# Performance work log

Measured on AMD Instinct MI355X. Metric: run time of the kernel, lower is better.

Reference implementation:

```python
import jax, jax.numpy as jnp
import numpy as np

T_, N_, DIN, D, HEADS, WW, E_, DPE = 8, 20000, 128, 128, 4, 4, 320000, 8
DH = D // HEADS
NEG = -1e30
EPS_GATE = 1e-6


def setup_inputs() -> dict:
    key = jax.random.key(0)
    ks = jax.random.split(key, 10)
    return {
        "H_tilde": jax.random.normal(ks[0], (T_, N_, DIN), jnp.float32),
        "S": jax.random.uniform(ks[1], (T_, N_), jnp.float32),
        "Wq": jax.random.normal(ks[2], (D, DIN), jnp.float32) * 0.05,
        "Wkh": jax.random.normal(ks[3], (D, DIN), jnp.float32) * 0.05,
        "Wkpe": jax.random.normal(ks[4], (D, DPE), jnp.float32) * 0.05,
        "Wv": jax.random.normal(ks[5], (D, DIN), jnp.float32) * 0.05,
        "pe_table": jax.random.normal(ks[6], (WW + 1, DPE), jnp.float32),
        "rel_bias": jax.random.normal(ks[7], (WW + 1,), jnp.float32),
        "src": jax.random.randint(ks[8], (E_,), 0, N_),
        "dst": jax.random.randint(ks[9], (E_,), 0, N_),
    }


def reference(H_tilde, S, Wq, Wkh, Wkpe, Wv, pe_table, rel_bias, src, dst):
    T, N, _ = H_tilde.shape
    H, dh, W = HEADS, DH, WW
    scale = dh ** -0.5
    dtype = H_tilde.dtype

    # Projections (torch Linear: x @ W.T). W_k over concat([H, pe]) splits additively.
    Q = (H_tilde @ Wq.T).reshape(T, N, H, dh)
    K0 = (H_tilde @ Wkh.T).reshape(T, N, H, dh)
    V = (H_tilde @ Wv.T).reshape(T, N, H, dh)
    pe_k = (pe_table @ Wkpe.T).reshape(W + 1, H, dh)
    gate = jnp.log(jnp.clip(S, 0.0, 1.0) + EPS_GATE)  # (T, N)

    # Pad W zero-steps in front so a length-(W+1) slice at t covers t-W..t.
    pad = lambda x: jnp.concatenate([jnp.zeros((W,) + x.shape[1:], x.dtype), x], axis=0)
    Kp, Vp, gp = pad(K0), pad(V), pad(gate)

    def step(_, tq):
        t, Qt = tq  # Qt: (N, H, dh)
        Kwin = jax.lax.dynamic_slice_in_dim(Kp, t, W + 1, 0)[::-1]  # (W+1,N,H,dh), dt=0..W
        Vwin = jax.lax.dynamic_slice_in_dim(Vp, t, W + 1, 0)[::-1]
        gwin = jax.lax.dynamic_slice_in_dim(gp, t, W + 1, 0)[::-1]  # (W+1, N)
        Qd = Qt[dst]  # (E, H, dh)

        scores = []
        for dt in range(W + 1):
            Ks = Kwin[dt][src] + pe_k[dt][None]  # (E, H, dh)
            s = (jnp.einsum('ehc,ehc->eh', Qd, Ks) * scale
                 + rel_bias[dt] + gwin[dt][src][:, None])
            scores.append(jnp.where(dt <= t, s, NEG))  # mask dt > t (W_eff = min(W, t))
        sc = jnp.stack(scores)  # (W+1, E, H)

        # Segment softmax over incoming edges of each dst node, jointly over dt.
        mx = jax.ops.segment_max(sc.transpose(1, 0, 2), dst, num_segments=N)  # (N,W+1,H)
        mx = mx.max(axis=1)  # (N, H)
        valid = (jnp.arange(W + 1) <= t)[:, None, None]
        ex = jnp.where(valid, jnp.exp(sc - mx[dst][None]), 0.0)  # (W+1, E, H)

        denom = jax.ops.segment_sum(ex.sum(axis=0), dst, num_segments=N)  # (N, H)
        numer = jnp.zeros((N, H, dh), dtype)
        for dt in range(W + 1):
            contrib = ex[dt][:, :, None] * Vwin[dt][src]  # (E, H, dh)
            numer = numer + jax.ops.segment_sum(contrib, dst, num_segments=N)

        msg = numer / jnp.maximum(denom, 1e-12)[:, :, None]  # (N, H, dh)
        return None, msg.reshape(N, H * dh)

    _, M_out = jax.lax.scan(step, None, (jnp.arange(T), Q))
    return M_out  # (T, N, d)
```

## Files before the change

### kernel.cpp

```cpp
#include <hip/hip_runtime.h>

typedef unsigned short u16;
typedef unsigned int u32;
typedef __attribute__((ext_vector_type(8))) __bf16 bf16x8;
typedef __attribute__((ext_vector_type(4))) float f32x4;
typedef __attribute__((ext_vector_type(4))) _Float16 f16x4;
typedef __attribute__((ext_vector_type(2))) unsigned u32x2;

constexpr int TT = 8, NN = 20000, DD = 128, EE = 320000;
constexpr int MAXDEG = 64;
constexpr float SCL = 0.17677669529663687f;
constexpr int VBLK = 272;

__device__ __forceinline__ u16 f2bf(float f) {
  u32 u = __float_as_uint(f);
  return (u16)((u + 0x7fffu + ((u >> 16) & 1u)) >> 16);
}
__device__ __forceinline__ u16 f2h(float f) {
  _Float16 h = (_Float16)f;
  return __builtin_bit_cast(unsigned short, h);
}
__device__ __forceinline__ float blo(u32 u) { return __uint_as_float(u << 16); }
__device__ __forceinline__ float bhi(u32 u) { return __uint_as_float(u & 0xffff0000u); }

__global__ void k_init(const float* __restrict__ pe_table, const float* __restrict__ Wkpe,
                       float* __restrict__ pek, int* __restrict__ cnt) {
  int i = blockIdx.x * 256 + threadIdx.x;
  if (i < NN) cnt[i] = 0;
  if (i < 5 * DD) {
    int dt = i >> 7, j = i & 127;
    float s = 0.f;
    for (int p = 0; p < 8; ++p) s += pe_table[dt * 8 + p] * Wkpe[j * 8 + p];
    pek[i] = s;
  }
}

__global__ void k_build(const int* __restrict__ src, const int* __restrict__ dst,
                        int* __restrict__ cnt, int* __restrict__ eslot) {
  int i = blockIdx.x * 256 + threadIdx.x;
  if (i < EE) {
    int d = dst[i];
    int p = atomicAdd(&cnt[d], 1);
    if (p < MAXDEG) eslot[d * MAXDEG + p] = src[i];
  }
}

__global__ __launch_bounds__(256) void k_proj3(
    const float* __restrict__ Hm, const float* __restrict__ Wq,
    const float* __restrict__ Wkh, const float* __restrict__ Wv,
    u16* __restrict__ Qb, u16* __restrict__ Kb, u16* __restrict__ Vb) {
  __shared__ u16 As[128 * 128];
  __shared__ u16 Bs[128 * 128];
  int tid = threadIdx.x;
  size_t m0 = (size_t)blockIdx.x * 128;

  for (int it = 0; it < 8; ++it) {
    int q = it * 256 + tid;
    int r = q >> 4, cb = q & 15;
    int sidx = r * 128 + ((cb ^ (r & 7)) << 3);
    const float* gp = Hm + (m0 + (size_t)r) * DD + cb * 8;
    float4 f0 = *(const float4*)gp;
    float4 f1 = *(const float4*)(gp + 4);
    u16 tmp[8] = {f2bf(f0.x), f2bf(f0.y), f2bf(f0.z), f2bf(f0.w),
                  f2bf(f1.x), f2bf(f1.y), f2bf(f1.z), f2bf(f1.w)};
    *(bf16x8*)(As + sidx) = *(const bf16x8*)tmp;
  }

  int lane = tid & 63, wv = tid >> 6;
  int wr = wv >> 1, wc = wv & 1;
  int l15 = lane & 15, lq = lane >> 4;

  for (int y = 0; y < 3; ++y) {
    const float* Wsel = (y == 0) ? Wq : (y == 1) ? Wkh : Wv;
    u16* Out = (y == 0) ? Qb : (y == 1) ? Kb : Vb;
    const bool asF16 = (y == 2);
    __syncthreads();
    for (int it = 0; it < 8; ++it) {
      int q = it * 256 + tid;
      int r = q >> 4, cb = q & 15;
      int sidx = r * 128 + ((cb ^ (r & 7)) << 3);
      const float* wp = Wsel + (size_t)r * DD + cb * 8;
      float4 f0 = *(const float4*)wp;
      float4 f1 = *(const float4*)(wp + 4);
      u16 tmp[8] = {f2bf(f0.x), f2bf(f0.y), f2bf(f0.z), f2bf(f0.w),
                    f2bf(f1.x), f2bf(f1.y), f2bf(f1.z), f2bf(f1.w)};
      *(bf16x8*)(Bs + sidx) = *(const bf16x8*)tmp;
    }
    __syncthreads();

    f32x4 acc[4][4];
    for (int i = 0; i < 4; ++i)
      for (int j = 0; j < 4; ++j) acc[i][j] = (f32x4){0.f, 0.f, 0.f, 0.f};

    for (int ks = 0; ks < 4; ++ks) {
      bf16x8 a[4], b[4];
      int cb = ks * 4 + lq;
      for (int i = 0; i < 4; ++i) {
        int r = wr * 64 + i * 16 + l15;
        a[i] = *(const bf16x8*)(As + r * 128 + ((cb ^ (r & 7)) << 3));
      }
      for (int j = 0; j < 4; ++j) {
        int r = wc * 64 + j * 16 + l15;
        b[j] = *(const bf16x8*)(Bs + r * 128 + ((cb ^ (r & 7)) << 3));
      }
      for (int i = 0; i < 4; ++i)
        for (int j = 0; j < 4; ++j)
          acc[i][j] = __builtin_amdgcn_mfma_f32_16x16x32_bf16(a[i], b[j], acc[i][j], 0, 0, 0);
    }

    for (int i = 0; i < 4; ++i)
      for (int j = 0; j < 4; ++j)
        for (int g = 0; g < 4; ++g) {
          size_t row = m0 + wr * 64 + i * 16 + lq * 4 + g;
          int col = wc * 64 + j * 16 + l15;
          Out[row * DD + col] = asF16 ? f2h(acc[i][j][g]) : f2bf(acc[i][j][g]);
        }
  }
}

__global__ __launch_bounds__(256) void k_etab(const u16* __restrict__ Qb,
                                              const float* __restrict__ pek,
                                              const float* __restrict__ relb,
                                              float* __restrict__ Etab) {
  int t = blockIdx.y;
  int n = blockIdx.x * 64 + (threadIdx.x >> 2);
  int h = threadIdx.x & 3;
  if (n >= NN) return;
  const u16* qp = Qb + ((size_t)t * NN + n) * DD + h * 32;
  float q[32];
#pragma unroll
  for (int u = 0; u < 4; ++u) {
    uint4 qv = *(const uint4*)(qp + u * 8);
    q[u*8+0]=blo(qv.x); q[u*8+1]=bhi(qv.x); q[u*8+2]=blo(qv.y); q[u*8+3]=bhi(qv.y);
    q[u*8+4]=blo(qv.z); q[u*8+5]=bhi(qv.z); q[u*8+6]=blo(qv.w); q[u*8+7]=bhi(qv.w);
  }
#pragma unroll
  for (int d = 0; d < 5; ++d) {
    float s = 0.f;
#pragma unroll
    for (int c = 0; c < 32; ++c) s += q[c] * pek[d * DD + h * 32 + c];
    Etab[((size_t)(t * 5 + d) * NN + n) * 4 + h] = __expf(s * SCL + relb[d]);
  }
}

struct KF { uint4 a, b, c, d; };
struct VF { uint4 a, b, c, d; };

__global__ __launch_bounds__(256, 3) void k_agg5(
    const u16* __restrict__ Qb, const u16* __restrict__ Kb, const u16* __restrict__ Vb,
    const float* __restrict__ Sarr, const float* __restrict__ Etab,
    const int* __restrict__ cnt, const int* __restrict__ eslot,
    float* __restrict__ outp) {
  __shared__ int srcS[4][MAXDEG];
  __shared__ float eS[4][40][4];
  __shared__ u16 VldsS[4][8 * VBLK];
  int tid = threadIdx.x;
  int wv = tid >> 6, lane = tid & 63;
  int n0 = blockIdx.x * 4;
  const int n = n0 + wv;

  for (int i = tid; i < 640; i += 256) {
    int p = i >> 4, nn = (i >> 2) & 3, hh = i & 3;
    eS[nn][p][hh] = Etab[((size_t)p * NN + (n0 + nn)) * 4 + hh];
  }
  int deg = min(cnt[n], MAXDEG);
  srcS[wv][lane] = (lane < deg) ? eslot[n * MAXDEG + lane] : 0;
  __syncthreads();

  const int t16 = lane & 15, qo = lane >> 4, qo4 = qo * 4;

  uint4 qb0, qb1, qb2, qb3;
  {
    bool qok = t16 < 8;
    const u16* Qp = Qb + ((size_t)(t16 & 7) * NN + n) * DD + qo * 8;
    uint4 zz = make_uint4(0u, 0u, 0u, 0u);
    qb0 = qok ? *(const uint4*)(Qp) : zz;
    qb1 = qok ? *(const uint4*)(Qp + 32) : zz;
    qb2 = qok ? *(const uint4*)(Qp + 64) : zz;
    qb3 = qok ? *(const uint4*)(Qp + 96) : zz;
  }

  f32x4 numer[4][2];
#pragma unroll
  for (int h = 0; h < 4; ++h) {
    numer[h][0] = (f32x4){0.f, 0.f, 0.f, 0.f};
    numer[h][1] = (f32x4){0.f, 0.f, 0.f, 0.f};
  }
  float dd[4] = {0.f, 0.f, 0.f, 0.f};

  if (deg > 0) {
    const int degm1 = deg - 1;
    const int nch = (deg + 15) >> 4;
    const int cmax = nch << 4;
    const int nj = nch * 8;

    u16* vbuf = &VldsS[wv][0];
    unsigned vb0 = (unsigned)(uintptr_t)vbuf;
    unsigned trbase = vb0 + lane * 8;
    unsigned wbase = ((unsigned)((lane & 15) >> 1)) * (VBLK * 2) + qo * 32 + (lane & 1) * 16;

    auto loadK = [&](int tp, int c16) -> KF {
      const u16* Kp = Kb + (size_t)tp * (NN * DD)
                    + (size_t)srcS[wv][min(c16 + t16, degm1)] * DD + qo * 8;
      KF f;
      f.a = *(const uint4*)(Kp);
      f.b = *(const uint4*)(Kp + 32);
      f.c = *(const uint4*)(Kp + 64);
      f.d = *(const uint4*)(Kp + 96);
      return f;
    };
    auto loadV = [&](int tp, int c16) -> VF {
      const u16* Vsl = Vb + (size_t)tp * (NN * DD);
      int cg8 = (lane & 15) * 8;
      VF f;
      f.a = *(const uint4*)(Vsl + (size_t)srcS[wv][min(c16 + qo, degm1)] * DD + cg8);
      f.b = *(const uint4*)(Vsl + (size_t)srcS[wv][min(c16 + 4 + qo, degm1)] * DD + cg8);
      f.c = *(const uint4*)(Vsl + (size_t)srcS[wv][min(c16 + 8 + qo, degm1)] * DD + cg8);
      f.d = *(const uint4*)(Vsl + (size_t)srcS[wv][min(c16 + 12 + qo, degm1)] * DD + cg8);
      return f;
    };
    auto loadSg = [&](int tp, int c16) -> float {
      float sgn = 0.f;
      if (lane < 16) {
        float s = Sarr[(size_t)tp * NN + srcS[wv][min(c16 + lane, degm1)]];
        sgn = fminf(fmaxf(s, 0.f), 1.f) + 1e-6f;
      }
      return sgn;
    };
    auto writeV = [&](VF f) {
      *(uint4*)((char*)vbuf + (wbase)) = f.a;
      *(uint4*)((char*)vbuf + (wbase + 128)) = f.b;
      *(uint4*)((char*)vbuf + (wbase + 256)) = f.c;
      *(uint4*)((char*)vbuf + (wbase + 384)) = f.d;
    };
    auto compute = [&](KF kf, float sg, int tp, int c16) {
      int dt = t16 - tp;
      bool tval = (dt >= 0) && (dt <= 4) && (t16 < 8);
      float Ef[4];
#pragma unroll
      for (int h = 0; h < 4; ++h)
        Ef[h] = tval ? eS[wv][t16 * 5 + dt][h] : 0.f;

      f32x4 z = (f32x4){0.f, 0.f, 0.f, 0.f};
      f32x4 sc[4];
      sc[0] = __builtin_amdgcn_mfma_f32_16x16x32_bf16(
          __builtin_bit_cast(bf16x8, kf.a), __builtin_bit_cast(bf16x8, qb0), z, 0, 0, 0);
      sc[1] = __builtin_amdgcn_mfma_f32_16x16x32_bf16(
          __builtin_bit_cast(bf16x8, kf.b), __builtin_bit_cast(bf16x8, qb1), z, 0, 0, 0);
      sc[2] = __builtin_amdgcn_mfma_f32_16x16x32_bf16(
          __builtin_bit_cast(bf16x8, kf.c), __builtin_bit_cast(bf16x8, qb2), z, 0, 0, 0);
      sc[3] = __builtin_amdgcn_mfma_f32_16x16x32_bf16(
          __builtin_bit_cast(bf16x8, kf.d), __builtin_bit_cast(bf16x8, qb3), z, 0, 0, 0);

      float sgm[4];
#pragma unroll
      for (int r = 0; r < 4; ++r) {
        float sgr = __shfl(sg, qo4 + r);
        sgm[r] = ((c16 + qo4 + r) < deg) ? sgr : 0.f;
      }
      f16x4 wf[4];
#pragma unroll
      for (int h = 0; h < 4; ++h) {
#pragma unroll
        for (int r = 0; r < 4; ++r) {
          float w = __expf(sc[h][r] * SCL) * Ef[h] * sgm[r];
          dd[h] += w;
          wf[h][r] = (_Float16)w;
        }
      }

      __builtin_amdgcn_sched_barrier(0);
      u32x2 vr[4][2];
#pragma unroll
      for (int h = 0; h < 4; ++h) {
#pragma unroll
        for (int tile = 0; tile < 2; ++tile) {
          unsigned a = trbase + (unsigned)(h * 2 + tile) * (VBLK * 2);
          asm volatile("ds_read_b64_tr_b16 %0, %1" : "=v"(vr[h][tile]) : "v"(a));
        }
      }
      asm volatile("s_waitcnt lgkmcnt(0)");
      __builtin_amdgcn_sched_barrier(0);
#pragma unroll
      for (int h = 0; h < 4; ++h) {
#pragma unroll
        for (int tile = 0; tile < 2; ++tile) {
          numer[h][tile] = __builtin_amdgcn_mfma_f32_16x16x16f16(
              wf[h], __builtin_bit_cast(f16x4, vr[h][tile]), numer[h][tile], 0, 0, 0);
        }
      }
    };

    KF kA = loadK(0, 0);
    float sgA = loadSg(0, 0);
    writeV(loadV(0, 0));
    int tpj = 0, cj = 0;
    int tpn = 0, cn = 16;
    if (cn >= cmax) { cn = 0; tpn = 1; }

    for (int j = 0; j < nj; ++j) {
      bool more = (j + 1) < nj;
      KF kB;
      VF vB;
      float sgB = 0.f;
      if (more) {
        kB = loadK(tpn, cn);
        vB = loadV(tpn, cn);
        sgB = loadSg(tpn, cn);
      }
      compute(kA, sgA, tpj, cj);
      __builtin_amdgcn_sched_barrier(0);
      if (more) writeV(vB);
      kA = kB;
      sgA = sgB;
      tpj = tpn; cj = cn;
      cn += 16;
      if (cn >= cmax) { cn = 0; ++tpn; }
    }
  }

#pragma unroll
  for (int h = 0; h < 4; ++h) {
    float Dh = dd[h];
    Dh += __shfl_xor(Dh, 16);
    Dh += __shfl_xor(Dh, 32);
#pragma unroll
    for (int r = 0; r < 4; ++r) {
      int t = qo4 + r;
      float Dt = __shfl(Dh, t);
      if (t < 8) {
        float inv = 1.f / fmaxf(Dt, 1e-12f);
        float* op = outp + ((size_t)t * NN + n) * DD + h * 32;
        op[t16] = numer[h][0][r] * inv;
        op[16 + t16] = numer[h][1][r] * inv;
      }
    }
  }
}

extern "C" void kernel_launch(void* const* d_in, const int* in_sizes, int n_in,
                              void* d_out, int out_size, void* d_ws, size_t ws_size,
                              hipStream_t stream) {
  const float* Hm = (const float*)d_in[0];
  const float* S = (const float*)d_in[1];
  const float* Wq = (const float*)d_in[2];
  const float* Wkh = (const float*)d_in[3];
  const float* Wkpe = (const float*)d_in[4];
  const float* Wv = (const float*)d_in[5];
  const float* pe_table = (const float*)d_in[6];
  const float* relb = (const float*)d_in[7];
  const int* src = (const int*)d_in[8];
  const int* dst = (const int*)d_in[9];
  float* out = (float*)d_out;

  auto aup = [](size_t x) { return (x + 255) & ~(size_t)255; };
  char* base = (char*)d_ws;
  size_t off = 0;
  u16* Qb = (u16*)(base + off); off = aup(off + (size_t)TT * NN * DD * 2);
  u16* Kb = (u16*)(base + off); off = aup(off + (size_t)TT * NN * DD * 2);
  u16* Vb = (u16*)(base + off); off = aup(off + (size_t)TT * NN * DD * 2);
  float* pek = (float*)(base + off); off = aup(off + (size_t)5 * DD * 4);
  float* Etab = (float*)(base + off); off = aup(off + (size_t)TT * 5 * NN * 4 * 4);
  int* cnt = (int*)(base + off); off = aup(off + (size_t)NN * 4);
  int* eslot = (int*)(base + off); off = aup(off + (size_t)NN * MAXDEG * 4);
  (void)ws_size; (void)in_sizes; (void)n_in; (void)out_size;

  k_init<<<(NN + 255) / 256, 256, 0, stream>>>(pe_table, Wkpe, pek, cnt);
  k_build<<<(EE + 255) / 256, 256, 0, stream>>>(src, dst, cnt, eslot);
  k_proj3<<<1250, 256, 0, stream>>>(Hm, Wq, Wkh, Wv, Qb, Kb, Vb);
  k_etab<<<dim3((NN + 63) / 64, TT), 256, 0, stream>>>(Qb, pek, relb, Etab);
  k_agg5<<<NN / 4, 256, 0, stream>>>(Qb, Kb, Vb, S, Etab, cnt, eslot, out);
}
```

Measured before the change: 342.8 us.

## Pre-convert weights, drop LDS staging in projection, triple-buffer aggregation prefetch

Weights are converted to bf16 once in the init kernel. The projection kernel then reads H and the weights straight from global memory into MFMA fragments, with no shared-memory staging and no barriers. The aggregation kernel moves from a double-buffered K/V/S prefetch to a three-stage rotation, giving more loads in flight. It also has each wave load its own Etab slice with a float4 read, removing a block barrier, and computes the gate on all lanes. The trade-offs are uncoalesced global reads in the projection, since each lane reads 32B rows and every wave rereads H, and higher register pressure in the aggregation kernel.

```diff
diff --git a/kernel.cpp b/kernel.cpp
--- a/kernel.cpp
+++ b/kernel.cpp
@@ -13,18 +13,26 @@
 constexpr int VBLK = 272;
 
 __device__ __forceinline__ u16 f2bf(float f) {
-  u32 u = __float_as_uint(f);
-  return (u16)((u + 0x7fffu + ((u >> 16) & 1u)) >> 16);
+  return __builtin_bit_cast(u16, (__bf16)f);
 }
 __device__ __forceinline__ u16 f2h(float f) {
-  _Float16 h = (_Float16)f;
-  return __builtin_bit_cast(unsigned short, h);
+  return __builtin_bit_cast(u16, (_Float16)f);
 }
 __device__ __forceinline__ float blo(u32 u) { return __uint_as_float(u << 16); }
 __device__ __forceinline__ float bhi(u32 u) { return __uint_as_float(u & 0xffff0000u); }
 
+__device__ __forceinline__ bf16x8 cvt8(float4 f0, float4 f1) {
+  bf16x8 r;
+  r[0] = (__bf16)f0.x; r[1] = (__bf16)f0.y; r[2] = (__bf16)f0.z; r[3] = (__bf16)f0.w;
+  r[4] = (__bf16)f1.x; r[5] = (__bf16)f1.y; r[6] = (__bf16)f1.z; r[7] = (__bf16)f1.w;
+  return r;
+}
+
 __global__ void k_init(const float* __restrict__ pe_table, const float* __restrict__ Wkpe,
-                       float* __restrict__ pek, int* __restrict__ cnt) {
+                       const float* __restrict__ Wq, const float* __restrict__ Wkh,
+                       const float* __restrict__ Wv,
+                       float* __restrict__ pek, int* __restrict__ cnt,
+                       u16* __restrict__ Wb) {
   int i = blockIdx.x * 256 + threadIdx.x;
   if (i < NN) cnt[i] = 0;
   if (i < 5 * DD) {
@@ -33,6 +41,11 @@
     for (int p = 0; p < 8; ++p) s += pe_table[dt * 8 + p] * Wkpe[j * 8 + p];
     pek[i] = s;
   }
+  if (i < 3 * DD * DD) {
+    int y = i / (DD * DD), idx = i % (DD * DD);
+    const float* W = (y == 0) ? Wq : (y == 1) ? Wkh : Wv;
+    Wb[i] = f2bf(W[idx]);
+  }
 }
 
 __global__ void k_build(const int* __restrict__ src, const int* __restrict__ dst,
@@ -45,71 +58,47 @@
   }
 }
 
-__global__ __launch_bounds__(256) void k_proj3(
-    const float* __restrict__ Hm, const float* __restrict__ Wq,
-    const float* __restrict__ Wkh, const float* __restrict__ Wv,
+__global__ __launch_bounds__(256) void k_proj5(
+    const float* __restrict__ Hm, const u16* __restrict__ Wb,
     u16* __restrict__ Qb, u16* __restrict__ Kb, u16* __restrict__ Vb) {
-  __shared__ u16 As[128 * 128];
-  __shared__ u16 Bs[128 * 128];
   int tid = threadIdx.x;
-  size_t m0 = (size_t)blockIdx.x * 128;
-
-  for (int it = 0; it < 8; ++it) {
-    int q = it * 256 + tid;
-    int r = q >> 4, cb = q & 15;
-    int sidx = r * 128 + ((cb ^ (r & 7)) << 3);
-    const float* gp = Hm + (m0 + (size_t)r) * DD + cb * 8;
-    float4 f0 = *(const float4*)gp;
-    float4 f1 = *(const float4*)(gp + 4);
-    u16 tmp[8] = {f2bf(f0.x), f2bf(f0.y), f2bf(f0.z), f2bf(f0.w),
-                  f2bf(f1.x), f2bf(f1.y), f2bf(f1.z), f2bf(f1.w)};
-    *(bf16x8*)(As + sidx) = *(const bf16x8*)tmp;
-  }
-
   int lane = tid & 63, wv = tid >> 6;
   int wr = wv >> 1, wc = wv & 1;
   int l15 = lane & 15, lq = lane >> 4;
+  size_t m0 = (size_t)blockIdx.x * 128;
 
   for (int y = 0; y < 3; ++y) {
-    const float* Wsel = (y == 0) ? Wq : (y == 1) ? Wkh : Wv;
     u16* Out = (y == 0) ? Qb : (y == 1) ? Kb : Vb;
     const bool asF16 = (y == 2);
-    __syncthreads();
-    for (int it = 0; it < 8; ++it) {
-      int q = it * 256 + tid;
-      int r = q >> 4, cb = q & 15;
-      int sidx = r * 128 + ((cb ^ (r & 7)) << 3);
-      const float* wp = Wsel + (size_t)r * DD + cb * 8;
-      float4 f0 = *(const float4*)wp;
-      float4 f1 = *(const float4*)(wp + 4);
-      u16 tmp[8] = {f2bf(f0.x), f2bf(f0.y), f2bf(f0.z), f2bf(f0.w),
-                    f2bf(f1.x), f2bf(f1.y), f2bf(f1.z), f2bf(f1.w)};
-      *(bf16x8*)(Bs + sidx) = *(const bf16x8*)tmp;
-    }
-    __syncthreads();
+    const u16* Wy = Wb + y * DD * DD;
 
     f32x4 acc[4][4];
     for (int i = 0; i < 4; ++i)
       for (int j = 0; j < 4; ++j) acc[i][j] = (f32x4){0.f, 0.f, 0.f, 0.f};
 
     for (int ks = 0; ks < 4; ++ks) {
+      int col0 = ks * 32 + lq * 8;
       bf16x8 a[4], b[4];
-      int cb = ks * 4 + lq;
+#pragma unroll
       for (int i = 0; i < 4; ++i) {
-        int r = wr * 64 + i * 16 + l15;
-        a[i] = *(const bf16x8*)(As + r * 128 + ((cb ^ (r & 7)) << 3));
-      }
-      for (int j = 0; j < 4; ++j) {
-        int r = wc * 64 + j * 16 + l15;
-        b[j] = *(const bf16x8*)(Bs + r * 128 + ((cb ^ (r & 7)) << 3));
-      }
+        const float* gp = Hm + (m0 + wr * 64 + i * 16 + l15) * DD + col0;
+        a[i] = cvt8(*(const float4*)gp, *(const float4*)(gp + 4));
+      }
+#pragma unroll
+      for (int j = 0; j < 4; ++j)
+        b[j] = *(const bf16x8*)(Wy + (wc * 64 + j * 16 + l15) * DD + col0);
+#pragma unroll
       for (int i = 0; i < 4; ++i)
+#pragma unroll
         for (int j = 0; j < 4; ++j)
           acc[i][j] = __builtin_amdgcn_mfma_f32_16x16x32_bf16(a[i], b[j], acc[i][j], 0, 0, 0);
     }
 
+#pragma unroll
     for (int i = 0; i < 4; ++i)
+#pragma unroll
       for (int j = 0; j < 4; ++j)
+#pragma unroll
         for (int g = 0; g < 4; ++g) {
           size_t row = m0 + wr * 64 + i * 16 + lq * 4 + g;
           int col = wc * 64 + j * 16 + l15;
@@ -146,7 +135,7 @@
 struct KF { uint4 a, b, c, d; };
 struct VF { uint4 a, b, c, d; };
 
-__global__ __launch_bounds__(256, 3) void k_agg5(
+__global__ __launch_bounds__(256, 3) void k_agg6(
     const u16* __restrict__ Qb, const u16* __restrict__ Kb, const u16* __restrict__ Vb,
     const float* __restrict__ Sarr, const float* __restrict__ Etab,
     const int* __restrict__ cnt, const int* __restrict__ eslot,
@@ -156,16 +145,12 @@
   __shared__ u16 VldsS[4][8 * VBLK];
   int tid = threadIdx.x;
   int wv = tid >> 6, lane = tid & 63;
-  int n0 = blockIdx.x * 4;
-  const int n = n0 + wv;
-
-  for (int i = tid; i < 640; i += 256) {
-    int p = i >> 4, nn = (i >> 2) & 3, hh = i & 3;
-    eS[nn][p][hh] = Etab[((size_t)p * NN + (n0 + nn)) * 4 + hh];
-  }
+  const int n = blockIdx.x * 4 + wv;
+
   int deg = min(cnt[n], MAXDEG);
   srcS[wv][lane] = (lane < deg) ? eslot[n * MAXDEG + lane] : 0;
-  __syncthreads();
+  if (lane < 40)
+    *(float4*)&eS[wv][lane][0] = *(const float4*)&Etab[((size_t)lane * NN + n) * 4];
 
   const int t16 = lane & 15, qo = lane >> 4, qo4 = qo * 4;
 
@@ -220,12 +205,8 @@
       return f;
     };
     auto loadSg = [&](int tp, int c16) -> float {
-      float sgn = 0.f;
-      if (lane < 16) {
-        float s = Sarr[(size_t)tp * NN + srcS[wv][min(c16 + lane, degm1)]];
-        sgn = fminf(fmaxf(s, 0.f), 1.f) + 1e-6f;
-      }
-      return sgn;
+      float s = Sarr[(size_t)tp * NN + srcS[wv][min(c16 + (lane & 15), degm1)]];
+      return fminf(fmaxf(s, 0.f), 1.f) + 1e-6f;
     };
     auto writeV = [&](VF f) {
       *(uint4*)((char*)vbuf + (wbase)) = f.a;
@@ -291,31 +272,39 @@
       }
     };
 
-    KF kA = loadK(0, 0);
-    float sgA = loadSg(0, 0);
-    writeV(loadV(0, 0));
-    int tpj = 0, cj = 0;
-    int tpn = 0, cn = 16;
-    if (cn >= cmax) { cn = 0; tpn = 1; }
-
-    for (int j = 0; j < nj; ++j) {
-      bool more = (j + 1) < nj;
-      KF kB;
-      VF vB;
-      float sgB = 0.f;
-      if (more) {
-        kB = loadK(tpn, cn);
-        vB = loadV(tpn, cn);
-        sgB = loadSg(tpn, cn);
-      }
-      compute(kA, sgA, tpj, cj);
-      __builtin_amdgcn_sched_barrier(0);
-      if (more) writeV(vB);
-      kA = kB;
-      sgA = sgB;
-      tpj = tpn; cj = cn;
-      cn += 16;
-      if (cn >= cmax) { cn = 0; ++tpn; }
+    auto adv = [&](int2 x) -> int2 {
+      x.y += 16;
+      if (x.y >= cmax) { x.y = 0; ++x.x; }
+      return x;
+    };
+
+    int2 icur = make_int2(0, 0);
+    int2 i1 = adv(icur);
+    int2 ifet = adv(i1);
+    KF kA = loadK(0, 0), kB, kC;
+    float gA = loadSg(0, 0), gB = 0.f, gC = 0.f;
+    VF vA, vB, vC;
+    { VF v0 = loadV(0, 0); writeV(v0); }
+    if (nj > 1) { kB = loadK(i1.x, i1.y); gB = loadSg(i1.x, i1.y); vB = loadV(i1.x, i1.y); }
+
+    for (int j = 0; j < nj; j += 3) {
+      if (j + 2 < nj) { kC = loadK(ifet.x, ifet.y); gC = loadSg(ifet.x, ifet.y);
+                        vC = loadV(ifet.x, ifet.y); ifet = adv(ifet); }
+      compute(kA, gA, icur.x, icur.y); icur = adv(icur);
+      __builtin_amdgcn_sched_barrier(0);
+      if (j + 1 < nj) writeV(vB);
+      if (j + 1 >= nj) break;
+      if (j + 3 < nj) { kA = loadK(ifet.x, ifet.y); gA = loadSg(ifet.x, ifet.y);
+                        vA = loadV(ifet.x, ifet.y); ifet = adv(ifet); }
+      compute(kB, gB, icur.x, icur.y); icur = adv(icur);
+      __builtin_amdgcn_sched_barrier(0);
+      if (j + 2 < nj) writeV(vC);
+      if (j + 2 >= nj) break;
+      if (j + 4 < nj) { kB = loadK(ifet.x, ifet.y); gB = loadSg(ifet.x, ifet.y);
+                        vB = loadV(ifet.x, ifet.y); ifet = adv(ifet); }
+      compute(kC, gC, icur.x, icur.y); icur = adv(icur);
+      __builtin_amdgcn_sched_barrier(0);
+      if (j + 3 < nj) writeV(vA);
     }
   }
 
@@ -363,11 +352,13 @@
   float* Etab = (float*)(base + off); off = aup(off + (size_t)TT * 5 * NN * 4 * 4);
   int* cnt = (int*)(base + off); off = aup(off + (size_t)NN * 4);
   int* eslot = (int*)(base + off); off = aup(off + (size_t)NN * MAXDEG * 4);
+  u16* Wb = (u16*)(base + off); off = aup(off + (size_t)3 * DD * DD * 2);
   (void)ws_size; (void)in_sizes; (void)n_in; (void)out_size;
 
-  k_init<<<(NN + 255) / 256, 256, 0, stream>>>(pe_table, Wkpe, pek, cnt);
+  k_init<<<(3 * DD * DD + 255) / 256, 256, 0, stream>>>(pe_table, Wkpe, Wq, Wkh, Wv,
+                                                        pek, cnt, Wb);
   k_build<<<(EE + 255) / 256, 256, 0, stream>>>(src, dst, cnt, eslot);
-  k_proj3<<<1250, 256, 0, stream>>>(Hm, Wq, Wkh, Wv, Qb, Kb, Vb);
+  k_proj5<<<1250, 256, 0, stream>>>(Hm, Wb, Qb, Kb, Vb);
   k_etab<<<dim3((NN + 63) / 64, TT), 256, 0, stream>>>(Qb, pek, relb, Etab);
-  k_agg5<<<NN / 4, 256, 0, stream>>>(Qb, Kb, Vb, S, Etab, cnt, eslot, out);
-}
+  k_agg6<<<NN / 4, 256, 0, stream>>>(Qb, Kb, Vb, S, Etab, cnt, eslot, out);
+}
```

After: 711.5 us. +107.5%, slower.
